# Kernel tuning notes

Measured on AMD Instinct MI355X. Metric: run time of the kernel, lower is better.

The kernel has to match this reference:

```python
import jax, jax.numpy as jnp
import numpy as np

NINP = 512
NHID = 512
INITRANGE = 0.04
# DARTS RNN genotype: list of (activation, predecessor state index); concat = mean of states 1..8
RECURRENT = [("tanh", 0), ("relu", 1), ("relu", 1), ("identity", 1), ("tanh", 2), ("sigmoid", 5), ("tanh", 3), ("relu", 5)]
CONCAT = list(range(1, 9))
ACT = {"tanh": jnp.tanh, "relu": jax.nn.relu, "sigmoid": jax.nn.sigmoid, "identity": lambda x: x}


def setup_inputs() -> dict:
    key = jax.random.key(0)
    k0, k1, k2 = jax.random.split(key, 3)
    T, B = 400, 256
    inputs = jax.random.normal(k0, (T, B, NINP), dtype=jnp.float32)
    hidden = jnp.zeros((1, B, NHID), dtype=jnp.float32)
    W0 = jax.random.uniform(k1, (NINP + NHID, 2 * NHID), jnp.float32, -INITRANGE, INITRANGE)
    Ws = jax.random.uniform(k2, (len(RECURRENT), NHID, 2 * NHID), jnp.float32, -INITRANGE, INITRANGE)
    return {"inputs": inputs, "hidden": hidden, "W0": W0, "Ws": Ws}


def _cell(x, h_prev, W0, Ws):
    # init state: highway gate from concat(x, h_prev) @ W0
    xh = jnp.concatenate([x, h_prev], axis=-1)            # [B, ninp+nhid]
    c0, h0 = jnp.split(xh @ W0, 2, axis=-1)               # each [B, nhid]
    s0 = h_prev + jax.nn.sigmoid(c0) * (jnp.tanh(h0) - h_prev)
    states = [s0]
    for i, (name, pred) in enumerate(RECURRENT):          # fixed small DAG
        sp = states[pred]
        c, h = jnp.split(sp @ Ws[i], 2, axis=-1)
        s = sp + jax.nn.sigmoid(c) * (ACT[name](h) - sp)
        states.append(s)
    return jnp.mean(jnp.stack([states[i] for i in CONCAT], axis=-1), axis=-1)


def reference(inputs, hidden, W0, Ws):
    h0 = hidden[0]                                        # [B, nhid]

    def step(h, x):
        h_new = _cell(x, h, W0, Ws)
        return h_new, h_new

    h_last, hiddens = jax.lax.scan(step, h0, inputs)      # hiddens: [T, B, nhid]
    return hiddens, h_last[None]
```

## Files before the change

### kernel.cpp

```cpp
#include <hip/hip_runtime.h>
#include <stdint.h>

typedef unsigned short ushort_t;
typedef unsigned long long u64;
typedef __attribute__((ext_vector_type(8))) short short8;
typedef __attribute__((ext_vector_type(4))) float f32x4;
typedef __attribute__((ext_vector_type(4))) unsigned int u32x4;
typedef __attribute__((ext_vector_type(16))) float f32x16;

#define WS_W0T_HI 0u
#define WS_W0T_LO (2u<<20)
#define WS_WST_HI (4u<<20)
#define WS_WST_LO (12u<<20)
#define WS_ST     (20u<<20)
#define WS_BAR    (26u<<20)

#define SLOT_ELEMS 262144
#define PLANE 131072
#define PSTR 536


__device__ __forceinline__ ushort_t f2bf(float f) {
  unsigned u = __float_as_uint(f);
  u += 0x7FFFu + ((u >> 16) & 1u);
  return (ushort_t)(u >> 16);
}
__device__ __forceinline__ float bf2f(ushort_t h) {
  return __uint_as_float(((unsigned)h) << 16);
}
__device__ __forceinline__ float sigf(float v) { return 1.f / (1.f + __expf(-v)); }

__device__ __forceinline__ u32x4 uld16(const void* p) {
  u32x4 r;
  asm volatile("global_load_dwordx4 %0, %1, off sc0 sc1" : "=v"(r) : "v"(p));
  return r;
}

__device__ __forceinline__ void st_state(ushort_t* slot, int eo, float s, int tid) {
  ushort_t hi = f2bf(s);
  ushort_t lo = f2bf(s - bf2f(hi));
  unsigned nh = __shfl_xor((unsigned)hi, 1, 64);
  unsigned nl = __shfl_xor((unsigned)lo, 1, 64);
  if (!(tid & 1)) {
    unsigned wh = (unsigned)hi | (nh << 16);
    unsigned wl = (unsigned)lo | (nl << 16);
    __hip_atomic_store((unsigned*)(slot + eo), wh, __ATOMIC_RELAXED, __HIP_MEMORY_SCOPE_AGENT);
    __hip_atomic_store((unsigned*)(slot + PLANE + eo), wl, __ATOMIC_RELAXED, __HIP_MEMORY_SCOPE_AGENT);
  }
}

__device__ __forceinline__ void xcvt(const float* xp, short8& ah, short8& al) {
  f32x4 v0 = *(const f32x4*)xp;
  f32x4 v1 = *(const f32x4*)(xp + 4);
#pragma unroll
  for (int i = 0; i < 4; ++i) {
    ushort_t h0 = f2bf(v0[i]);
    ah[i] = (short)h0; al[i] = (short)f2bf(v0[i] - bf2f(h0));
    ushort_t h1 = f2bf(v1[i]);
    ah[i + 4] = (short)h1; al[i + 4] = (short)f2bf(v1[i] - bf2f(h1));
  }
}

extern "C" __global__ void prep_kernel(const float* __restrict__ W0,
                                       const float* __restrict__ Ws,
                                       const float* __restrict__ h0,
                                       char* __restrict__ ws) {
  ushort_t* w0h = (ushort_t*)(ws + WS_W0T_HI);
  ushort_t* w0l = (ushort_t*)(ws + WS_W0T_LO);
  ushort_t* wsh = (ushort_t*)(ws + WS_WST_HI);
  ushort_t* wsl = (ushort_t*)(ws + WS_WST_LO);
  ushort_t* st  = (ushort_t*)(ws + WS_ST);
  const long N0 = 1048576, N1 = 4194304, N2 = 131072;
  long total = N0 + N1 + N2;
  for (long idx = (long)blockIdx.x * blockDim.x + threadIdx.x; idx < total;
       idx += (long)gridDim.x * blockDim.x) {
    if (idx < N0) {
      int k = (int)(idx >> 10), j = (int)(idx & 1023);
      float v = W0[k * 1024 + j];
      ushort_t hi = f2bf(v);
      w0h[j * 1024 + k] = hi;
      w0l[j * 1024 + k] = f2bf(v - bf2f(hi));
    } else if (idx < N0 + N1) {
      long r = idx - N0;
      int i = (int)(r >> 19);
      int r2 = (int)(r & 524287);
      int k = r2 >> 10, j = r2 & 1023;
      float v = Ws[(long)i * 524288 + k * 1024 + j];
      ushort_t hi = f2bf(v);
      wsh[(long)i * 524288 + j * 512 + k] = hi;
      wsl[(long)i * 524288 + j * 512 + k] = f2bf(v - bf2f(hi));
    } else {
      int e = (int)(idx - N0 - N1);
      float v = h0[e];
      ushort_t hi = f2bf(v);
      st[0 * SLOT_ELEMS + e] = hi;
      st[0 * SLOT_ELEMS + PLANE + e] = f2bf(v - bf2f(hi));
    }
  }
}

__device__ __forceinline__ void set_flag(unsigned* flags, int g, int pt, unsigned gen) {
  __syncthreads();
  if (threadIdx.x == 0)
    __hip_atomic_store(flags + (g * 32 + pt) * 16, gen, __ATOMIC_RELAXED, __HIP_MEMORY_SCOPE_AGENT);
}

__device__ __forceinline__ void panel_load(const ushort_t* slot, int r0,
                                           ushort_t* Ah, ushort_t* Al,
                                           const unsigned* flags, int g, unsigned G,
                                           int tid) {
  const int row = tid >> 4, c0 = (tid & 15) * 32;
  const int p0 = (tid & 15) * 2;
  const unsigned* f0 = flags + (g * 32 + p0) * 16;
  const unsigned* f1 = flags + (g * 32 + p0 + 1) * 16;
  while (__hip_atomic_load(f0, __ATOMIC_RELAXED, __HIP_MEMORY_SCOPE_AGENT) < G)
    __builtin_amdgcn_s_sleep(2);
  while (__hip_atomic_load(f1, __ATOMIC_RELAXED, __HIP_MEMORY_SCOPE_AGENT) < G)
    __builtin_amdgcn_s_sleep(2);
  const ushort_t* srch = slot + (r0 + row) * 512 + c0;
  u32x4 v[8];
#pragma unroll
  for (int j = 0; j < 4; ++j) v[j] = uld16(srch + j * 8);
#pragma unroll
  for (int j = 0; j < 4; ++j) v[4 + j] = uld16(srch + PLANE + j * 8);
  asm volatile("s_waitcnt vmcnt(0)" ::: "memory");
  __builtin_amdgcn_sched_barrier(0);
#pragma unroll
  for (int j = 0; j < 4; ++j) {
    *(u32x4*)(Ah + row * PSTR + c0 + j * 8) = v[j];
    *(u32x4*)(Al + row * PSTR + c0 + j * 8) = v[4 + j];
  }
}

__device__ __forceinline__ f32x16 mfma3(short8 ah, short8 al, short8 bh, short8 bl, f32x16 acc) {
  acc = __builtin_amdgcn_mfma_f32_32x32x16_bf16(ah, bh, acc, 0, 0, 0);
  acc = __builtin_amdgcn_mfma_f32_32x32x16_bf16(ah, bl, acc, 0, 0, 0);
  acc = __builtin_amdgcn_mfma_f32_32x32x16_bf16(al, bh, acc, 0, 0, 0);
  return acc;
}

template<int NP, int NBLK, bool XA>
__device__ __forceinline__ void mm_lds(const ushort_t* Ah, const ushort_t* Al,
                                       const float* xrow,
                                       const ushort_t* const (&bh)[NP],
                                       const ushort_t* const (&bl)[NP],
                                       int boff, int kw, int lr,
                                       f32x16 (&acc)[NP]) {
#pragma unroll
  for (int j = 0; j < NBLK; ++j) {
    int kq = j * 128 + kw;
    short8 a_h, a_l;
    if (XA && j < 4) {
      xcvt(xrow + kq, a_h, a_l);
    } else {
      int kp = XA ? (kq - 512) : kq;
      a_h = *(const short8*)(Ah + lr * PSTR + kp);
      a_l = *(const short8*)(Al + lr * PSTR + kp);
    }
#pragma unroll
    for (int p = 0; p < NP; ++p) {
      short8 b_h = *(const short8*)(bh[p] + boff + kq);
      short8 b_l = *(const short8*)(bl[p] + boff + kq);
      acc[p] = mfma3(a_h, a_l, b_h, b_l, acc[p]);
    }
  }
}

__device__ __forceinline__ void wr_pp1(float* pp, const f32x16& a, int w, int lane) {
  int col = lane & 31, h5 = lane >> 5;
  float* base = pp + w * 1056 + col;
#pragma unroll
  for (int r = 0; r < 16; ++r) {
    int row = (r & 3) + 8 * (r >> 2) + 4 * h5;
    base[row * 33] = a[r];
  }
}
__device__ __forceinline__ void rd_pp1(const float* pp, int row, int cp,
                                       float& c, float& h) {
  float cs = 0.f, hs = 0.f;
#pragma unroll
  for (int w = 0; w < 8; ++w) {
    cs += pp[w * 1056 + row * 33 + cp];
    hs += pp[w * 1056 + row * 33 + cp + 16];
  }
  c = cs; h = hs;
}

extern "C" __global__ void __launch_bounds__(512, 1)
rnn_main(const float* __restrict__ x, float* __restrict__ out, char* __restrict__ ws) {
  __shared__ ushort_t Ah[32 * PSTR];
  __shared__ ushort_t Al[32 * PSTR];
  __shared__ float pp[8 * 1056];

  ushort_t* stg = (ushort_t*)(ws + WS_ST);
  unsigned* flags = (unsigned*)(ws + WS_BAR);
  const ushort_t* w0h = (const ushort_t*)(ws + WS_W0T_HI);
  const ushort_t* w0l = (const ushort_t*)(ws + WS_W0T_LO);
  const ushort_t* wsh = (const ushort_t*)(ws + WS_WST_HI);
  const ushort_t* wsl = (const ushort_t*)(ws + WS_WST_LO);

  const int tid = threadIdx.x;
  const int wg = blockIdx.x;
  const int rt = wg >> 5, pt = wg & 31;
  const int g = rt, r0 = rt * 32;
  const int w = tid >> 6, lane = tid & 63;
  const int kw = w * 16 + (lane >> 5) * 8;
  const int lr = lane & 31;
  const int jc = pt * 16 + (lr & 15) + (lr >> 4) * 512;
  const int b512 = jc * 512, b1024 = jc * 1024;
  const int erow = tid >> 4, ecp = tid & 15;
  const int scol = pt * 16 + ecp;
  const int eo = (r0 + erow) * 512 + scol;
  const int spo = erow * PSTR + scol;

  float sumreg = 0.f;

  for (int t = 0; t < 400; ++t) {
    const unsigned base = 5u * (unsigned)t;
    const float* xrow = x + (size_t)t * 131072 + (size_t)(r0 + lr) * 512;

    panel_load(stg + 0 * SLOT_ELEMS, r0, Ah, Al, flags, g, base, tid);
    __syncthreads();
    {
      f32x16 acc[1] = {};
      const ushort_t* bh[1] = {w0h};
      const ushort_t* bl[1] = {w0l};
      mm_lds<1, 8, true>(Ah, Al, xrow, bh, bl, b1024, kw, lr, acc);
      __syncthreads();
      wr_pp1(pp, acc[0], w, lane);
      __syncthreads();
      float c, hh; rd_pp1(pp, erow, ecp, c, hh);
      float sp = bf2f(Ah[spo]) + bf2f(Al[spo]);
      float s = sp + sigf(c) * (tanhf(hh) - sp);
      st_state(stg + 1 * SLOT_ELEMS, eo, s, tid);
    }
    set_flag(flags, g, pt, base + 1);

    panel_load(stg + 1 * SLOT_ELEMS, r0, Ah, Al, flags, g, base + 1, tid);
    __syncthreads();
    {
      f32x16 acc[1] = {};
      const ushort_t* bh[1] = {wsh + 0 * 524288};
      const ushort_t* bl[1] = {wsl + 0 * 524288};
      mm_lds<1, 4, false>(Ah, Al, nullptr, bh, bl, b512, kw, lr, acc);
      __syncthreads();
      wr_pp1(pp, acc[0], w, lane);
      __syncthreads();
      float c, hh; rd_pp1(pp, erow, ecp, c, hh);
      float sp = bf2f(Ah[spo]) + bf2f(Al[spo]);
      float s = sp + sigf(c) * (tanhf(hh) - sp);
      sumreg += s;
      st_state(stg + 2 * SLOT_ELEMS, eo, s, tid);
    }
    set_flag(flags, g, pt, base + 2);

    panel_load(stg + 2 * SLOT_ELEMS, r0, Ah, Al, flags, g, base + 2, tid);
    __syncthreads();
    {
      f32x16 acc[3] = {};
      const ushort_t* bh[3] = {wsh + 1 * 524288, wsh + 2 * 524288, wsh + 3 * 524288};
      const ushort_t* bl[3] = {wsl + 1 * 524288, wsl + 2 * 524288, wsl + 3 * 524288};
      mm_lds<3, 4, false>(Ah, Al, nullptr, bh, bl, b512, kw, lr, acc);
      float sp;
      __syncthreads();
      wr_pp1(pp, acc[0], w, lane);
      __syncthreads();
      {
        float c, hh; rd_pp1(pp, erow, ecp, c, hh);
        sp = bf2f(Ah[spo]) + bf2f(Al[spo]);
        float s = sp + sigf(c) * (fmaxf(hh, 0.f) - sp);
        sumreg += s;
        st_state(stg + 3 * SLOT_ELEMS, eo, s, tid);
      }
      __syncthreads();
      wr_pp1(pp, acc[1], w, lane);
      __syncthreads();
      {
        float c, hh; rd_pp1(pp, erow, ecp, c, hh);
        float s = sp + sigf(c) * (fmaxf(hh, 0.f) - sp);
        sumreg += s;
        st_state(stg + 4 * SLOT_ELEMS, eo, s, tid);
      }
      set_flag(flags, g, pt, base + 3);
      wr_pp1(pp, acc[2], w, lane);
      __syncthreads();
      {
        float c, hh; rd_pp1(pp, erow, ecp, c, hh);
        sumreg += sp + sigf(c) * (hh - sp);
      }
    }

    __syncthreads();
    panel_load(stg + 3 * SLOT_ELEMS, r0, Ah, Al, flags, g, base + 3, tid);
    __syncthreads();
    {
      f32x16 acc[1] = {};
      const ushort_t* bh[1] = {wsh + 4 * 524288};
      const ushort_t* bl[1] = {wsl + 4 * 524288};
      mm_lds<1, 4, false>(Ah, Al, nullptr, bh, bl, b512, kw, lr, acc);
      __syncthreads();
      wr_pp1(pp, acc[0], w, lane);
      __syncthreads();
      float c, hh; rd_pp1(pp, erow, ecp, c, hh);
      float sp = bf2f(Ah[spo]) + bf2f(Al[spo]);
      float s = sp + sigf(c) * (tanhf(hh) - sp);
      sumreg += s;
      st_state(stg + 5 * SLOT_ELEMS, eo, s, tid);
    }
    set_flag(flags, g, pt, base + 4);

    panel_load(stg + 4 * SLOT_ELEMS, r0, Ah, Al, flags, g, base + 3, tid);
    __syncthreads();
    {
      f32x16 acc[1] = {};
      const ushort_t* bh[1] = {wsh + 6 * 524288};
      const ushort_t* bl[1] = {wsl + 6 * 524288};
      mm_lds<1, 4, false>(Ah, Al, nullptr, bh, bl, b512, kw, lr, acc);
      __syncthreads();
      wr_pp1(pp, acc[0], w, lane);
      __syncthreads();
      float c, hh; rd_pp1(pp, erow, ecp, c, hh);
      float sp = bf2f(Ah[spo]) + bf2f(Al[spo]);
      sumreg += sp + sigf(c) * (tanhf(hh) - sp);
    }

    __syncthreads();
    panel_load(stg + 5 * SLOT_ELEMS, r0, Ah, Al, flags, g, base + 4, tid);
    __syncthreads();
    {
      f32x16 acc[2] = {};
      const ushort_t* bh[2] = {wsh + 5 * 524288, wsh + 7 * 524288};
      const ushort_t* bl[2] = {wsl + 5 * 524288, wsl + 7 * 524288};
      mm_lds<2, 4, false>(Ah, Al, nullptr, bh, bl, b512, kw, lr, acc);
      __syncthreads();
      wr_pp1(pp, acc[0], w, lane);
      __syncthreads();
      float sp = bf2f(Ah[spo]) + bf2f(Al[spo]);
      {
        float c, hh; rd_pp1(pp, erow, ecp, c, hh);
        sumreg += sp + sigf(c) * (sigf(hh) - sp);
      }
      __syncthreads();
      wr_pp1(pp, acc[1], w, lane);
      __syncthreads();
      {
        float c, hh; rd_pp1(pp, erow, ecp, c, hh);
        sumreg += sp + sigf(c) * (fmaxf(hh, 0.f) - sp);
      }
      float hn = sumreg * 0.125f;
      __builtin_nontemporal_store(hn, &out[(size_t)t * 131072 + eo]);
      if (t == 399)
        __builtin_nontemporal_store(hn, &out[(size_t)400 * 131072 + eo]);
      st_state(stg + 0 * SLOT_ELEMS, eo, hn, tid);
      sumreg = 0.f;
    }
    set_flag(flags, g, pt, base + 5);
  }
}

extern "C" void kernel_launch(void* const* d_in, const int* in_sizes, int n_in,
                              void* d_out, int out_size, void* d_ws, size_t ws_size,
                              hipStream_t stream) {
  const float* x  = (const float*)d_in[0];
  const float* h0 = (const float*)d_in[1];
  const float* W0 = (const float*)d_in[2];
  const float* Ws = (const float*)d_in[3];
  float* out = (float*)d_out;
  char* ws = (char*)d_ws;

  (void)in_sizes; (void)n_in; (void)out_size; (void)ws_size;

  (void)hipMemsetAsync(ws + WS_BAR, 0, 16384, stream);
  hipLaunchKernelGGL(prep_kernel, dim3(2048), dim3(256), 0, stream, W0, Ws, h0, ws);

  void* args[3] = {(void*)&x, (void*)&out, (void*)&ws};
  (void)hipLaunchCooperativeKernel((void*)rnn_main, dim3(256), dim3(512), args, 0, stream);
}
```

Baseline: 17.77 ms.

## Merge states 5 and 7 matmuls into one dual-panel pass with split K halves

The two independent DAG nodes fed by states 2 and 3 (Ws[4] and Ws[6]) now share a single flag wait and panel load. Both panels are split into K halves that are staged through the existing LDS buffers, and the global loads for the second half are issued while the first half's MFMAs run. This removes one full panel-load/barrier round and overlaps memory latency with compute. The panel_load flag mapping and column layout also change to match the half-split ordering. The cost is more complex LDS reuse with extra syncs and more live registers.

```diff
diff --git a/kernel.cpp b/kernel.cpp
--- a/kernel.cpp
+++ b/kernel.cpp
@@ -18,6 +18,7 @@
 #define SLOT_ELEMS 262144
 #define PLANE 131072
 #define PSTR 536
+#define PSTR2 268
 
 
 __device__ __forceinline__ ushort_t f2bf(float f) {
@@ -109,27 +110,26 @@
                                            ushort_t* Ah, ushort_t* Al,
                                            const unsigned* flags, int g, unsigned G,
                                            int tid) {
-  const int row = tid >> 4, c0 = (tid & 15) * 32;
-  const int p0 = (tid & 15) * 2;
-  const unsigned* f0 = flags + (g * 32 + p0) * 16;
-  const unsigned* f1 = flags + (g * 32 + p0 + 1) * 16;
+  const int row = tid >> 4, i = tid & 15;
+  const unsigned* f0 = flags + (g * 32 + i) * 16;
+  const unsigned* f1 = flags + (g * 32 + 16 + i) * 16;
   while (__hip_atomic_load(f0, __ATOMIC_RELAXED, __HIP_MEMORY_SCOPE_AGENT) < G)
     __builtin_amdgcn_s_sleep(2);
   while (__hip_atomic_load(f1, __ATOMIC_RELAXED, __HIP_MEMORY_SCOPE_AGENT) < G)
     __builtin_amdgcn_s_sleep(2);
-  const ushort_t* srch = slot + (r0 + row) * 512 + c0;
-  u32x4 v[8];
-#pragma unroll
-  for (int j = 0; j < 4; ++j) v[j] = uld16(srch + j * 8);
-#pragma unroll
-  for (int j = 0; j < 4; ++j) v[4 + j] = uld16(srch + PLANE + j * 8);
+  const ushort_t* src = slot + (r0 + row) * 512;
+  const int c0 = i * 16, c1 = 256 + i * 16;
+  u32x4 v0 = uld16(src + c0), v1 = uld16(src + c0 + 8);
+  u32x4 v2 = uld16(src + c1), v3 = uld16(src + c1 + 8);
+  u32x4 v4 = uld16(src + PLANE + c0), v5 = uld16(src + PLANE + c0 + 8);
+  u32x4 v6 = uld16(src + PLANE + c1), v7 = uld16(src + PLANE + c1 + 8);
   asm volatile("s_waitcnt vmcnt(0)" ::: "memory");
   __builtin_amdgcn_sched_barrier(0);
-#pragma unroll
-  for (int j = 0; j < 4; ++j) {
-    *(u32x4*)(Ah + row * PSTR + c0 + j * 8) = v[j];
-    *(u32x4*)(Al + row * PSTR + c0 + j * 8) = v[4 + j];
-  }
+  const int o0 = row * PSTR + c0, o1 = row * PSTR + c1;
+  *(u32x4*)(Ah + o0) = v0; *(u32x4*)(Ah + o0 + 8) = v1;
+  *(u32x4*)(Ah + o1) = v2; *(u32x4*)(Ah + o1 + 8) = v3;
+  *(u32x4*)(Al + o0) = v4; *(u32x4*)(Al + o0 + 8) = v5;
+  *(u32x4*)(Al + o1) = v6; *(u32x4*)(Al + o1 + 8) = v7;
 }
 
 __device__ __forceinline__ f32x16 mfma3(short8 ah, short8 al, short8 bh, short8 bl, f32x16 acc) {
@@ -166,6 +166,31 @@
   }
 }
 
+__device__ __forceinline__ void mmD(const ushort_t* B2, const ushort_t* B3,
+                                    const ushort_t* wah, const ushort_t* wal,
+                                    const ushort_t* wbh, const ushort_t* wbl,
+                                    int b512, int h, int w, int lane,
+                                    f32x16& acc5, f32x16& acc7) {
+  const int lr = lane & 31;
+  const int bkk = (lane >> 5) * 8;
+  const int ak = lr * PSTR2 + bkk;
+#pragma unroll
+  for (int s = 0; s < 2; ++s) {
+    const int kl = w * 32 + s * 16;
+    const int kq = h * 256 + kl + bkk;
+    short8 a2h = *(const short8*)(B2 + ak + kl);
+    short8 a2l = *(const short8*)(B2 + 8576 + ak + kl);
+    short8 a3h = *(const short8*)(B3 + ak + kl);
+    short8 a3l = *(const short8*)(B3 + 8576 + ak + kl);
+    short8 bah = *(const short8*)(wah + b512 + kq);
+    short8 bal = *(const short8*)(wal + b512 + kq);
+    short8 bbh = *(const short8*)(wbh + b512 + kq);
+    short8 bbl = *(const short8*)(wbl + b512 + kq);
+    acc5 = mfma3(a2h, a2l, bah, bal, acc5);
+    acc7 = mfma3(a3h, a3l, bbh, bbl, acc7);
+  }
+}
+
 __device__ __forceinline__ void wr_pp1(float* pp, const f32x16& a, int w, int lane) {
   int col = lane & 31, h5 = lane >> 5;
   float* base = pp + w * 1056 + col;
@@ -188,8 +213,8 @@
 
 extern "C" __global__ void __launch_bounds__(512, 1)
 rnn_main(const float* __restrict__ x, float* __restrict__ out, char* __restrict__ ws) {
-  __shared__ ushort_t Ah[32 * PSTR];
-  __shared__ ushort_t Al[32 * PSTR];
+  __shared__ __align__(16) ushort_t Ah[32 * PSTR];
+  __shared__ __align__(16) ushort_t Al[32 * PSTR];
   __shared__ float pp[8 * 1056];
 
   ushort_t* stg = (ushort_t*)(ws + WS_ST);
@@ -290,38 +315,76 @@
       }
     }
 
-    __syncthreads();
-    panel_load(stg + 3 * SLOT_ELEMS, r0, Ah, Al, flags, g, base + 3, tid);
-    __syncthreads();
     {
-      f32x16 acc[1] = {};
-      const ushort_t* bh[1] = {wsh + 4 * 524288};
-      const ushort_t* bl[1] = {wsl + 4 * 524288};
-      mm_lds<1, 4, false>(Ah, Al, nullptr, bh, bl, b512, kw, lr, acc);
-      __syncthreads();
-      wr_pp1(pp, acc[0], w, lane);
-      __syncthreads();
-      float c, hh; rd_pp1(pp, erow, ecp, c, hh);
-      float sp = bf2f(Ah[spo]) + bf2f(Al[spo]);
-      float s = sp + sigf(c) * (tanhf(hh) - sp);
-      sumreg += s;
-      st_state(stg + 5 * SLOT_ELEMS, eo, s, tid);
-    }
-    set_flag(flags, g, pt, base + 4);
-
-    panel_load(stg + 4 * SLOT_ELEMS, r0, Ah, Al, flags, g, base + 3, tid);
-    __syncthreads();
-    {
-      f32x16 acc[1] = {};
-      const ushort_t* bh[1] = {wsh + 6 * 524288};
-      const ushort_t* bl[1] = {wsl + 6 * 524288};
-      mm_lds<1, 4, false>(Ah, Al, nullptr, bh, bl, b512, kw, lr, acc);
-      __syncthreads();
-      wr_pp1(pp, acc[0], w, lane);
-      __syncthreads();
-      float c, hh; rd_pp1(pp, erow, ecp, c, hh);
-      float sp = bf2f(Ah[spo]) + bf2f(Al[spo]);
-      sumreg += sp + sigf(c) * (tanhf(hh) - sp);
+      const int i = tid & 15;
+      const unsigned G3 = base + 3;
+      const unsigned* f0 = flags + (g * 32 + i) * 16;
+      const unsigned* f1 = flags + (g * 32 + 16 + i) * 16;
+      while (__hip_atomic_load(f0, __ATOMIC_RELAXED, __HIP_MEMORY_SCOPE_AGENT) < G3)
+        __builtin_amdgcn_s_sleep(2);
+      while (__hip_atomic_load(f1, __ATOMIC_RELAXED, __HIP_MEMORY_SCOPE_AGENT) < G3)
+        __builtin_amdgcn_s_sleep(2);
+      const int prow = tid >> 4;
+      const ushort_t* s2p = stg + 3 * SLOT_ELEMS + (r0 + prow) * 512;
+      const ushort_t* s3p = stg + 4 * SLOT_ELEMS + (r0 + prow) * 512;
+      const int po = prow * PSTR2 + i * 16;
+      {
+        u32x4 v0 = uld16(s2p + i * 16),        v1 = uld16(s2p + i * 16 + 8);
+        u32x4 v2 = uld16(s2p + PLANE + i * 16), v3 = uld16(s2p + PLANE + i * 16 + 8);
+        u32x4 q0 = uld16(s3p + i * 16),        q1 = uld16(s3p + i * 16 + 8);
+        u32x4 q2 = uld16(s3p + PLANE + i * 16), q3 = uld16(s3p + PLANE + i * 16 + 8);
+        asm volatile("s_waitcnt vmcnt(0)" ::: "memory");
+        __builtin_amdgcn_sched_barrier(0);
+        *(u32x4*)(Ah + po) = v0;        *(u32x4*)(Ah + po + 8) = v1;
+        *(u32x4*)(Ah + 8576 + po) = v2; *(u32x4*)(Ah + 8576 + po + 8) = v3;
+        *(u32x4*)(Al + po) = q0;        *(u32x4*)(Al + po + 8) = q1;
+        *(u32x4*)(Al + 8576 + po) = q2; *(u32x4*)(Al + 8576 + po + 8) = q3;
+      }
+      __syncthreads();
+      const int hstar = pt >> 4;
+      const int lcs = erow * PSTR2 + ((pt & 15) * 16 + ecp);
+      float sp2 = 0.f, sp3 = 0.f;
+      if (hstar == 0) {
+        sp2 = bf2f(Ah[lcs]) + bf2f(Ah[8576 + lcs]);
+        sp3 = bf2f(Al[lcs]) + bf2f(Al[8576 + lcs]);
+      }
+      u32x4 y0 = uld16(s2p + 256 + i * 16),        y1 = uld16(s2p + 256 + i * 16 + 8);
+      u32x4 y2 = uld16(s2p + PLANE + 256 + i * 16), y3 = uld16(s2p + PLANE + 256 + i * 16 + 8);
+      u32x4 z0 = uld16(s3p + 256 + i * 16),        z1 = uld16(s3p + 256 + i * 16 + 8);
+      u32x4 z2 = uld16(s3p + PLANE + 256 + i * 16), z3 = uld16(s3p + PLANE + 256 + i * 16 + 8);
+      f32x16 acc5 = {}, acc7 = {};
+      mmD(Ah, Al, wsh + 4 * 524288, wsl + 4 * 524288,
+          wsh + 6 * 524288, wsl + 6 * 524288, b512, 0, w, lane, acc5, acc7);
+      __syncthreads();
+      asm volatile("s_waitcnt vmcnt(0)" ::: "memory");
+      __builtin_amdgcn_sched_barrier(0);
+      *(u32x4*)(Ah + po) = y0;        *(u32x4*)(Ah + po + 8) = y1;
+      *(u32x4*)(Ah + 8576 + po) = y2; *(u32x4*)(Ah + 8576 + po + 8) = y3;
+      *(u32x4*)(Al + po) = z0;        *(u32x4*)(Al + po + 8) = z1;
+      *(u32x4*)(Al + 8576 + po) = z2; *(u32x4*)(Al + 8576 + po + 8) = z3;
+      __syncthreads();
+      if (hstar == 1) {
+        sp2 = bf2f(Ah[lcs]) + bf2f(Ah[8576 + lcs]);
+        sp3 = bf2f(Al[lcs]) + bf2f(Al[8576 + lcs]);
+      }
+      mmD(Ah, Al, wsh + 4 * 524288, wsl + 4 * 524288,
+          wsh + 6 * 524288, wsl + 6 * 524288, b512, 1, w, lane, acc5, acc7);
+      __syncthreads();
+      wr_pp1(pp, acc5, w, lane);
+      __syncthreads();
+      {
+        float c, hh; rd_pp1(pp, erow, ecp, c, hh);
+        float s5v = sp2 + sigf(c) * (tanhf(hh) - sp2);
+        sumreg += s5v;
+        st_state(stg + 5 * SLOT_ELEMS, eo, s5v, tid);
+      }
+      set_flag(flags, g, pt, base + 4);
+      wr_pp1(pp, acc7, w, lane);
+      __syncthreads();
+      {
+        float c, hh; rd_pp1(pp, erow, ecp, c, hh);
+        sumreg += sp3 + sigf(c) * (tanhf(hh) - sp3);
+      }
     }
 
     __syncthreads();
```

Result: slower. 20.02 ms (+12.7%).

## Retile recurrent cell to 16-row groups with per-wave K slices and MFMA-tiled weights

Applied to the files above, without the earlier changes.

Reorganises the persistent RNN kernel from 8 groups of 32 batch rows to 16 groups of 16 rows, each workgroup owning 32 output columns. Each wave now loads only its own 64-wide K slice of the state, gated by per-wave flag polling instead of a whole-panel wait. Weights are pre-swizzled into 16x16x32 MFMA tile order so operand loads are contiguous. The x-part of the first GEMM is computed before polling, states are kept in registers instead of being re-read from LDS, and the s3/s4 consumers are merged into one phase to cut barriers. The cost is more flag traffic, more workgroups per group synchronisation, and smaller MFMA tiles.

```diff
diff --git a/kernel.cpp b/kernel.cpp
--- a/kernel.cpp
+++ b/kernel.cpp
@@ -6,7 +6,6 @@
 typedef __attribute__((ext_vector_type(8))) short short8;
 typedef __attribute__((ext_vector_type(4))) float f32x4;
 typedef __attribute__((ext_vector_type(4))) unsigned int u32x4;
-typedef __attribute__((ext_vector_type(16))) float f32x16;
 
 #define WS_W0T_HI 0u
 #define WS_W0T_LO (2u<<20)
@@ -17,7 +16,7 @@
 
 #define SLOT_ELEMS 262144
 #define PLANE 131072
-#define PSTR 536
+#define SLW 72
 
 
 __device__ __forceinline__ ushort_t f2bf(float f) {
@@ -78,8 +77,10 @@
       int k = (int)(idx >> 10), j = (int)(idx & 1023);
       float v = W0[k * 1024 + j];
       ushort_t hi = f2bf(v);
-      w0h[j * 1024 + k] = hi;
-      w0l[j * 1024 + k] = f2bf(v - bf2f(hi));
+      long dst = ((long)(j >> 4) * 32 + (k >> 5)) * 512 +
+                 (((k >> 3) & 3) * 16 + (j & 15)) * 8 + (k & 7);
+      w0h[dst] = hi;
+      w0l[dst] = f2bf(v - bf2f(hi));
     } else if (idx < N0 + N1) {
       long r = idx - N0;
       int i = (int)(r >> 19);
@@ -87,8 +88,10 @@
       int k = r2 >> 10, j = r2 & 1023;
       float v = Ws[(long)i * 524288 + k * 1024 + j];
       ushort_t hi = f2bf(v);
-      wsh[(long)i * 524288 + j * 512 + k] = hi;
-      wsl[(long)i * 524288 + j * 512 + k] = f2bf(v - bf2f(hi));
+      long dst = (long)i * 524288 + ((long)(j >> 4) * 16 + (k >> 5)) * 512 +
+                 (((k >> 3) & 3) * 16 + (j & 15)) * 8 + (k & 7);
+      wsh[dst] = hi;
+      wsl[dst] = f2bf(v - bf2f(hi));
     } else {
       int e = (int)(idx - N0 - N1);
       float v = h0[e];
@@ -102,95 +105,88 @@
 __device__ __forceinline__ void set_flag(unsigned* flags, int g, int pt, unsigned gen) {
   __syncthreads();
   if (threadIdx.x == 0)
-    __hip_atomic_store(flags + (g * 32 + pt) * 16, gen, __ATOMIC_RELAXED, __HIP_MEMORY_SCOPE_AGENT);
-}
-
-__device__ __forceinline__ void panel_load(const ushort_t* slot, int r0,
-                                           ushort_t* Ah, ushort_t* Al,
-                                           const unsigned* flags, int g, unsigned G,
-                                           int tid) {
-  const int row = tid >> 4, c0 = (tid & 15) * 32;
-  const int p0 = (tid & 15) * 2;
-  const unsigned* f0 = flags + (g * 32 + p0) * 16;
-  const unsigned* f1 = flags + (g * 32 + p0 + 1) * 16;
-  while (__hip_atomic_load(f0, __ATOMIC_RELAXED, __HIP_MEMORY_SCOPE_AGENT) < G)
-    __builtin_amdgcn_s_sleep(2);
-  while (__hip_atomic_load(f1, __ATOMIC_RELAXED, __HIP_MEMORY_SCOPE_AGENT) < G)
-    __builtin_amdgcn_s_sleep(2);
-  const ushort_t* srch = slot + (r0 + row) * 512 + c0;
-  u32x4 v[8];
-#pragma unroll
-  for (int j = 0; j < 4; ++j) v[j] = uld16(srch + j * 8);
-#pragma unroll
-  for (int j = 0; j < 4; ++j) v[4 + j] = uld16(srch + PLANE + j * 8);
+    __hip_atomic_store(flags + (g * 16 + pt) * 16, gen, __ATOMIC_RELAXED, __HIP_MEMORY_SCOPE_AGENT);
+}
+__device__ __forceinline__ void pollw(const unsigned* flags, int g, int q0,
+                                      unsigned G, int lane) {
+  if (lane < 2) {
+    const unsigned* f = flags + (g * 16 + q0 + lane) * 16;
+    while (__hip_atomic_load(f, __ATOMIC_RELAXED, __HIP_MEMORY_SCOPE_AGENT) < G)
+      __builtin_amdgcn_s_sleep(2);
+  }
+}
+
+__device__ __forceinline__ void slice_load(const ushort_t* slot, int r0, int k0,
+                                           ushort_t* SlH, ushort_t* SlL, int lane) {
+  const int row = lane >> 3, part = lane & 7;
+  const ushort_t* s = slot + (r0 + row) * 512 + k0 + part * 8;
+  u32x4 a0 = uld16(s);
+  u32x4 a1 = uld16(s + 8 * 512);
+  u32x4 b0 = uld16(s + PLANE);
+  u32x4 b1 = uld16(s + PLANE + 8 * 512);
   asm volatile("s_waitcnt vmcnt(0)" ::: "memory");
   __builtin_amdgcn_sched_barrier(0);
-#pragma unroll
-  for (int j = 0; j < 4; ++j) {
-    *(u32x4*)(Ah + row * PSTR + c0 + j * 8) = v[j];
-    *(u32x4*)(Al + row * PSTR + c0 + j * 8) = v[4 + j];
-  }
-}
-
-__device__ __forceinline__ f32x16 mfma3(short8 ah, short8 al, short8 bh, short8 bl, f32x16 acc) {
-  acc = __builtin_amdgcn_mfma_f32_32x32x16_bf16(ah, bh, acc, 0, 0, 0);
-  acc = __builtin_amdgcn_mfma_f32_32x32x16_bf16(ah, bl, acc, 0, 0, 0);
-  acc = __builtin_amdgcn_mfma_f32_32x32x16_bf16(al, bh, acc, 0, 0, 0);
+  *(u32x4*)(SlH + row * SLW + part * 8) = a0;
+  *(u32x4*)(SlH + (row + 8) * SLW + part * 8) = a1;
+  *(u32x4*)(SlL + row * SLW + part * 8) = b0;
+  *(u32x4*)(SlL + (row + 8) * SLW + part * 8) = b1;
+}
+
+__device__ __forceinline__ f32x4 mfma3_4(short8 ah, short8 al, short8 bh, short8 bl, f32x4 acc) {
+  acc = __builtin_amdgcn_mfma_f32_16x16x32_bf16(ah, bh, acc, 0, 0, 0);
+  acc = __builtin_amdgcn_mfma_f32_16x16x32_bf16(ah, bl, acc, 0, 0, 0);
+  acc = __builtin_amdgcn_mfma_f32_16x16x32_bf16(al, bh, acc, 0, 0, 0);
   return acc;
 }
 
-template<int NP, int NBLK, bool XA>
-__device__ __forceinline__ void mm_lds(const ushort_t* Ah, const ushort_t* Al,
-                                       const float* xrow,
-                                       const ushort_t* const (&bh)[NP],
-                                       const ushort_t* const (&bl)[NP],
-                                       int boff, int kw, int lr,
-                                       f32x16 (&acc)[NP]) {
-#pragma unroll
-  for (int j = 0; j < NBLK; ++j) {
-    int kq = j * 128 + kw;
-    short8 a_h, a_l;
-    if (XA && j < 4) {
-      xcvt(xrow + kq, a_h, a_l);
-    } else {
-      int kp = XA ? (kq - 512) : kq;
-      a_h = *(const short8*)(Ah + lr * PSTR + kp);
-      a_l = *(const short8*)(Al + lr * PSTR + kp);
-    }
-#pragma unroll
-    for (int p = 0; p < NP; ++p) {
-      short8 b_h = *(const short8*)(bh[p] + boff + kq);
-      short8 b_l = *(const short8*)(bl[p] + boff + kq);
-      acc[p] = mfma3(a_h, a_l, b_h, b_l, acc[p]);
-    }
-  }
-}
-
-__device__ __forceinline__ void wr_pp1(float* pp, const f32x16& a, int w, int lane) {
-  int col = lane & 31, h5 = lane >> 5;
-  float* base = pp + w * 1056 + col;
-#pragma unroll
-  for (int r = 0; r < 16; ++r) {
-    int row = (r & 3) + 8 * (r >> 2) + 4 * h5;
-    base[row * 33] = a[r];
-  }
-}
-__device__ __forceinline__ void rd_pp1(const float* pp, int row, int cp,
-                                       float& c, float& h) {
+template<int NP>
+__device__ __forceinline__ void mm_slice(const ushort_t* SlH, const ushort_t* SlL,
+                                         const ushort_t* const (&wh)[NP],
+                                         const ushort_t* const (&wl)[NP],
+                                         const int (&jbs)[4], int KB, int kbg0,
+                                         int lane, f32x4 (&acc)[NP][4]) {
+#pragma unroll
+  for (int kb = 0; kb < 2; ++kb) {
+    const int ao = (lane & 15) * SLW + kb * 32 + (lane >> 4) * 8;
+    short8 ah = *(const short8*)(SlH + ao);
+    short8 al = *(const short8*)(SlL + ao);
+#pragma unroll
+    for (int p = 0; p < NP; ++p)
+#pragma unroll
+      for (int ct = 0; ct < 4; ++ct) {
+        const int tile = (jbs[ct] * KB + kbg0 + kb) * 512 + lane * 8;
+        short8 bh = *(const short8*)(wh[p] + tile);
+        short8 bl = *(const short8*)(wl[p] + tile);
+        acc[p][ct] = mfma3_4(ah, al, bh, bl, acc[p][ct]);
+      }
+  }
+}
+
+__device__ __forceinline__ void wrpp(float* pp, int m, const f32x4 (&a)[4], int w, int lane) {
+  const int col = lane & 15, rb = (lane >> 4) * 4;
+#pragma unroll
+  for (int ct = 0; ct < 4; ++ct) {
+    float* b = pp + (((m * 8 + w) * 4 + ct) * 16) * 16 + col;
+#pragma unroll
+    for (int r = 0; r < 4; ++r) b[(rb + r) * 16] = a[ct][r];
+  }
+}
+__device__ __forceinline__ void rdpp(const float* pp, int m, int row, int cl,
+                                     float& c, float& h) {
+  const int ctc = cl >> 4, col = cl & 15;
   float cs = 0.f, hs = 0.f;
 #pragma unroll
   for (int w = 0; w < 8; ++w) {
-    cs += pp[w * 1056 + row * 33 + cp];
-    hs += pp[w * 1056 + row * 33 + cp + 16];
+    cs += pp[(((m * 8 + w) * 4 + ctc) * 16 + row) * 16 + col];
+    hs += pp[(((m * 8 + w) * 4 + ctc + 2) * 16 + row) * 16 + col];
   }
   c = cs; h = hs;
 }
 
 extern "C" __global__ void __launch_bounds__(512, 1)
 rnn_main(const float* __restrict__ x, float* __restrict__ out, char* __restrict__ ws) {
-  __shared__ ushort_t Ah[32 * PSTR];
-  __shared__ ushort_t Al[32 * PSTR];
-  __shared__ float pp[8 * 1056];
+  __shared__ __align__(16) ushort_t Sl[8][2][16 * SLW];
+  __shared__ __align__(16) float pp[2 * 8 * 4 * 16 * 16];
 
   ushort_t* stg = (ushort_t*)(ws + WS_ST);
   unsigned* flags = (unsigned*)(ws + WS_BAR);
@@ -201,158 +197,156 @@
 
   const int tid = threadIdx.x;
   const int wg = blockIdx.x;
-  const int rt = wg >> 5, pt = wg & 31;
-  const int g = rt, r0 = rt * 32;
+  const int g = wg >> 4, pt = wg & 15;
+  const int r0 = g * 16;
   const int w = tid >> 6, lane = tid & 63;
-  const int kw = w * 16 + (lane >> 5) * 8;
-  const int lr = lane & 31;
-  const int jc = pt * 16 + (lr & 15) + (lr >> 4) * 512;
-  const int b512 = jc * 512, b1024 = jc * 1024;
-  const int erow = tid >> 4, ecp = tid & 15;
-  const int scol = pt * 16 + ecp;
-  const int eo = (r0 + erow) * 512 + scol;
-  const int spo = erow * PSTR + scol;
-
-  float sumreg = 0.f;
+  ushort_t* SlH = &Sl[w][0][0];
+  ushort_t* SlL = &Sl[w][1][0];
+  const int jbs[4] = {2 * pt, 2 * pt + 1, 32 + 2 * pt, 33 + 2 * pt};
+  const int q0 = 2 * w;
+  const int k0 = w * 64;
+
+  const int erow = tid >> 5, ecl = tid & 31;
+  const int eo = (r0 + erow) * 512 + pt * 32 + ecl;
+
+  float h_reg = bf2f(stg[eo]) + bf2f(stg[PLANE + eo]);
+  float s0_r = 0.f, s1_r = 0.f, s2_r = 0.f, s3_r = 0.f, s5_r = 0.f, sum = 0.f;
 
   for (int t = 0; t < 400; ++t) {
     const unsigned base = 5u * (unsigned)t;
-    const float* xrow = x + (size_t)t * 131072 + (size_t)(r0 + lr) * 512;
-
-    panel_load(stg + 0 * SLOT_ELEMS, r0, Ah, Al, flags, g, base, tid);
-    __syncthreads();
-    {
-      f32x16 acc[1] = {};
-      const ushort_t* bh[1] = {w0h};
-      const ushort_t* bl[1] = {w0l};
-      mm_lds<1, 8, true>(Ah, Al, xrow, bh, bl, b1024, kw, lr, acc);
-      __syncthreads();
-      wr_pp1(pp, acc[0], w, lane);
-      __syncthreads();
-      float c, hh; rd_pp1(pp, erow, ecp, c, hh);
-      float sp = bf2f(Ah[spo]) + bf2f(Al[spo]);
-      float s = sp + sigf(c) * (tanhf(hh) - sp);
-      st_state(stg + 1 * SLOT_ELEMS, eo, s, tid);
+
+    {
+      f32x4 acc[1][4] = {};
+      const float* xr = x + (size_t)t * 131072 + (size_t)(r0 + (lane & 15)) * 512
+                        + k0 + (lane >> 4) * 8;
+#pragma unroll
+      for (int kb = 0; kb < 2; ++kb) {
+        short8 ah, al; xcvt(xr + kb * 32, ah, al);
+#pragma unroll
+        for (int ct = 0; ct < 4; ++ct) {
+          const int tile = (jbs[ct] * 32 + q0 + kb) * 512 + lane * 8;
+          short8 bh = *(const short8*)(w0h + tile);
+          short8 bl = *(const short8*)(w0l + tile);
+          acc[0][ct] = mfma3_4(ah, al, bh, bl, acc[0][ct]);
+        }
+      }
+      pollw(flags, g, q0, base, lane);
+      slice_load(stg + 0 * SLOT_ELEMS, r0, k0, SlH, SlL, lane);
+      const ushort_t* wh1[1] = {w0h};
+      const ushort_t* wl1[1] = {w0l};
+      mm_slice<1>(SlH, SlL, wh1, wl1, jbs, 32, 16 + q0, lane, acc);
+      wrpp(pp, 0, acc[0], w, lane);
+      __syncthreads();
+      float c, hh; rdpp(pp, 0, erow, ecl, c, hh);
+      s0_r = h_reg + sigf(c) * (tanhf(hh) - h_reg);
+      st_state(stg + 1 * SLOT_ELEMS, eo, s0_r, tid);
     }
     set_flag(flags, g, pt, base + 1);
 
-    panel_load(stg + 1 * SLOT_ELEMS, r0, Ah, Al, flags, g, base + 1, tid);
-    __syncthreads();
-    {
-      f32x16 acc[1] = {};
-      const ushort_t* bh[1] = {wsh + 0 * 524288};
-      const ushort_t* bl[1] = {wsl + 0 * 524288};
-      mm_lds<1, 4, false>(Ah, Al, nullptr, bh, bl, b512, kw, lr, acc);
-      __syncthreads();
-      wr_pp1(pp, acc[0], w, lane);
-      __syncthreads();
-      float c, hh; rd_pp1(pp, erow, ecp, c, hh);
-      float sp = bf2f(Ah[spo]) + bf2f(Al[spo]);
-      float s = sp + sigf(c) * (tanhf(hh) - sp);
-      sumreg += s;
-      st_state(stg + 2 * SLOT_ELEMS, eo, s, tid);
+    {
+      pollw(flags, g, q0, base + 1, lane);
+      slice_load(stg + 1 * SLOT_ELEMS, r0, k0, SlH, SlL, lane);
+      f32x4 acc[1][4] = {};
+      const ushort_t* wh1[1] = {wsh + 0 * 524288};
+      const ushort_t* wl1[1] = {wsl + 0 * 524288};
+      mm_slice<1>(SlH, SlL, wh1, wl1, jbs, 16, q0, lane, acc);
+      wrpp(pp, 0, acc[0], w, lane);
+      __syncthreads();
+      float c, hh; rdpp(pp, 0, erow, ecl, c, hh);
+      s1_r = s0_r + sigf(c) * (tanhf(hh) - s0_r);
+      sum = s1_r;
+      st_state(stg + 2 * SLOT_ELEMS, eo, s1_r, tid);
     }
     set_flag(flags, g, pt, base + 2);
 
-    panel_load(stg + 2 * SLOT_ELEMS, r0, Ah, Al, flags, g, base + 2, tid);
-    __syncthreads();
-    {
-      f32x16 acc[3] = {};
-      const ushort_t* bh[3] = {wsh + 1 * 524288, wsh + 2 * 524288, wsh + 3 * 524288};
-      const ushort_t* bl[3] = {wsl + 1 * 524288, wsl + 2 * 524288, wsl + 3 * 524288};
-      mm_lds<3, 4, false>(Ah, Al, nullptr, bh, bl, b512, kw, lr, acc);
-      float sp;
-      __syncthreads();
-      wr_pp1(pp, acc[0], w, lane);
-      __syncthreads();
-      {
-        float c, hh; rd_pp1(pp, erow, ecp, c, hh);
-        sp = bf2f(Ah[spo]) + bf2f(Al[spo]);
-        float s = sp + sigf(c) * (fmaxf(hh, 0.f) - sp);
-        sumreg += s;
-        st_state(stg + 3 * SLOT_ELEMS, eo, s, tid);
-      }
-      __syncthreads();
-      wr_pp1(pp, acc[1], w, lane);
-      __syncthreads();
-      {
-        float c, hh; rd_pp1(pp, erow, ecp, c, hh);
-        float s = sp + sigf(c) * (fmaxf(hh, 0.f) - sp);
-        sumreg += s;
-        st_state(stg + 4 * SLOT_ELEMS, eo, s, tid);
-      }
+    {
+      pollw(flags, g, q0, base + 2, lane);
+      slice_load(stg + 2 * SLOT_ELEMS, r0, k0, SlH, SlL, lane);
+      f32x4 acc[3][4] = {};
+      const ushort_t* wh3[3] = {wsh + 1 * 524288, wsh + 2 * 524288, wsh + 3 * 524288};
+      const ushort_t* wl3[3] = {wsl + 1 * 524288, wsl + 2 * 524288, wsl + 3 * 524288};
+      mm_slice<3>(SlH, SlL, wh3, wl3, jbs, 16, q0, lane, acc);
+      wrpp(pp, 0, acc[0], w, lane);
+      wrpp(pp, 1, acc[1], w, lane);
+      __syncthreads();
+      float c, hh;
+      rdpp(pp, 0, erow, ecl, c, hh);
+      s2_r = s1_r + sigf(c) * (fmaxf(hh, 0.f) - s1_r);
+      sum += s2_r;
+      st_state(stg + 3 * SLOT_ELEMS, eo, s2_r, tid);
+      rdpp(pp, 1, erow, ecl, c, hh);
+      s3_r = s1_r + sigf(c) * (fmaxf(hh, 0.f) - s1_r);
+      sum += s3_r;
+      st_state(stg + 4 * SLOT_ELEMS, eo, s3_r, tid);
       set_flag(flags, g, pt, base + 3);
-      wr_pp1(pp, acc[2], w, lane);
-      __syncthreads();
-      {
-        float c, hh; rd_pp1(pp, erow, ecp, c, hh);
-        sumreg += sp + sigf(c) * (hh - sp);
-      }
-    }
-
-    __syncthreads();
-    panel_load(stg + 3 * SLOT_ELEMS, r0, Ah, Al, flags, g, base + 3, tid);
-    __syncthreads();
-    {
-      f32x16 acc[1] = {};
-      const ushort_t* bh[1] = {wsh + 4 * 524288};
-      const ushort_t* bl[1] = {wsl + 4 * 524288};
-      mm_lds<1, 4, false>(Ah, Al, nullptr, bh, bl, b512, kw, lr, acc);
-      __syncthreads();
-      wr_pp1(pp, acc[0], w, lane);
-      __syncthreads();
-      float c, hh; rd_pp1(pp, erow, ecp, c, hh);
-      float sp = bf2f(Ah[spo]) + bf2f(Al[spo]);
-      float s = sp + sigf(c) * (tanhf(hh) - sp);
-      sumreg += s;
-      st_state(stg + 5 * SLOT_ELEMS, eo, s, tid);
+      wrpp(pp, 0, acc[2], w, lane);
+      __syncthreads();
+      rdpp(pp, 0, erow, ecl, c, hh);
+      sum += s1_r + sigf(c) * (hh - s1_r);
+      __syncthreads();
+    }
+
+    {
+      pollw(flags, g, q0, base + 3, lane);
+      const int row = lane >> 3, part = lane & 7;
+      const ushort_t* p2 = stg + 3 * SLOT_ELEMS + (r0 + row) * 512 + k0 + part * 8;
+      const ushort_t* p3 = stg + 4 * SLOT_ELEMS + (r0 + row) * 512 + k0 + part * 8;
+      u32x4 a0 = uld16(p2), a1 = uld16(p2 + 8 * 512);
+      u32x4 a2 = uld16(p2 + PLANE), a3 = uld16(p2 + PLANE + 8 * 512);
+      u32x4 c0 = uld16(p3), c1 = uld16(p3 + 8 * 512);
+      u32x4 c2 = uld16(p3 + PLANE), c3 = uld16(p3 + PLANE + 8 * 512);
+      asm volatile("s_waitcnt vmcnt(4)" ::: "memory");
+      __builtin_amdgcn_sched_barrier(0);
+      *(u32x4*)(SlH + row * SLW + part * 8) = a0;
+      *(u32x4*)(SlH + (row + 8) * SLW + part * 8) = a1;
+      *(u32x4*)(SlL + row * SLW + part * 8) = a2;
+      *(u32x4*)(SlL + (row + 8) * SLW + part * 8) = a3;
+      f32x4 acc5[1][4] = {}, acc7[1][4] = {};
+      const ushort_t* wh4[1] = {wsh + 4 * 524288};
+      const ushort_t* wl4[1] = {wsl + 4 * 524288};
+      mm_slice<1>(SlH, SlL, wh4, wl4, jbs, 16, q0, lane, acc5);
+      asm volatile("s_waitcnt vmcnt(0)" ::: "memory");
+      __builtin_amdgcn_sched_barrier(0);
+      *(u32x4*)(SlH + row * SLW + part * 8) = c0;
+      *(u32x4*)(SlH + (row + 8) * SLW + part * 8) = c1;
+      *(u32x4*)(SlL + row * SLW + part * 8) = c2;
+      *(u32x4*)(SlL + (row + 8) * SLW + part * 8) = c3;
+      const ushort_t* wh6[1] = {wsh + 6 * 524288};
+      const ushort_t* wl6[1] = {wsl + 6 * 524288};
+      mm_slice<1>(SlH, SlL, wh6, wl6, jbs, 16, q0, lane, acc7);
+      wrpp(pp, 0, acc5[0], w, lane);
+      wrpp(pp, 1, acc7[0], w, lane);
+      __syncthreads();
+      float c, hh;
+      rdpp(pp, 0, erow, ecl, c, hh);
+      s5_r = s2_r + sigf(c) * (tanhf(hh) - s2_r);
+      sum += s5_r;
+      st_state(stg + 5 * SLOT_ELEMS, eo, s5_r, tid);
+      rdpp(pp, 1, erow, ecl, c, hh);
+      sum += s3_r + sigf(c) * (tanhf(hh) - s3_r);
     }
     set_flag(flags, g, pt, base + 4);
 
-    panel_load(stg + 4 * SLOT_ELEMS, r0, Ah, Al, flags, g, base + 3, tid);
-    __syncthreads();
-    {
-      f32x16 acc[1] = {};
-      const ushort_t* bh[1] = {wsh + 6 * 524288};
-      const ushort_t* bl[1] = {wsl + 6 * 524288};
-      mm_lds<1, 4, false>(Ah, Al, nullptr, bh, bl, b512, kw, lr, acc);
-      __syncthreads();
-      wr_pp1(pp, acc[0], w, lane);
-      __syncthreads();
-      float c, hh; rd_pp1(pp, erow, ecp, c, hh);
-      float sp = bf2f(Ah[spo]) + bf2f(Al[spo]);
-      sumreg += sp + sigf(c) * (tanhf(hh) - sp);
-    }
-
-    __syncthreads();
-    panel_load(stg + 5 * SLOT_ELEMS, r0, Ah, Al, flags, g, base + 4, tid);
-    __syncthreads();
-    {
-      f32x16 acc[2] = {};
-      const ushort_t* bh[2] = {wsh + 5 * 524288, wsh + 7 * 524288};
-      const ushort_t* bl[2] = {wsl + 5 * 524288, wsl + 7 * 524288};
-      mm_lds<2, 4, false>(Ah, Al, nullptr, bh, bl, b512, kw, lr, acc);
-      __syncthreads();
-      wr_pp1(pp, acc[0], w, lane);
-      __syncthreads();
-      float sp = bf2f(Ah[spo]) + bf2f(Al[spo]);
-      {
-        float c, hh; rd_pp1(pp, erow, ecp, c, hh);
-        sumreg += sp + sigf(c) * (sigf(hh) - sp);
-      }
-      __syncthreads();
-      wr_pp1(pp, acc[1], w, lane);
-      __syncthreads();
-      {
-        float c, hh; rd_pp1(pp, erow, ecp, c, hh);
-        sumreg += sp + sigf(c) * (fmaxf(hh, 0.f) - sp);
-      }
-      float hn = sumreg * 0.125f;
-      __builtin_nontemporal_store(hn, &out[(size_t)t * 131072 + eo]);
+    {
+      pollw(flags, g, q0, base + 4, lane);
+      slice_load(stg + 5 * SLOT_ELEMS, r0, k0, SlH, SlL, lane);
+      f32x4 acc[2][4] = {};
+      const ushort_t* wh2[2] = {wsh + 5 * 524288, wsh + 7 * 524288};
+      const ushort_t* wl2[2] = {wsl + 5 * 524288, wsl + 7 * 524288};
+      mm_slice<2>(SlH, SlL, wh2, wl2, jbs, 16, q0, lane, acc);
+      wrpp(pp, 0, acc[0], w, lane);
+      wrpp(pp, 1, acc[1], w, lane);
+      __syncthreads();
+      float c, hh;
+      rdpp(pp, 0, erow, ecl, c, hh);
+      sum += s5_r + sigf(c) * (sigf(hh) - s5_r);
+      rdpp(pp, 1, erow, ecl, c, hh);
+      sum += s5_r + sigf(c) * (fmaxf(hh, 0.f) - s5_r);
+      h_reg = sum * 0.125f;
+      __builtin_nontemporal_store(h_reg, &out[(size_t)t * 131072 + eo]);
       if (t == 399)
-        __builtin_nontemporal_store(hn, &out[(size_t)400 * 131072 + eo]);
-      st_state(stg + 0 * SLOT_ELEMS, eo, hn, tid);
-      sumreg = 0.f;
+        __builtin_nontemporal_store(h_reg, &out[(size_t)400 * 131072 + eo]);
+      st_state(stg + 0 * SLOT_ELEMS, eo, h_reg, tid);
     }
     set_flag(flags, g, pt, base + 5);
   }
@@ -370,7 +364,7 @@
 
   (void)in_sizes; (void)n_in; (void)out_size; (void)ws_size;
 
-  (void)hipMemsetAsync(ws + WS_BAR, 0, 16384, stream);
+  (void)hipMemsetAsync(ws + WS_BAR, 0, 32768, stream);
   hipLaunchKernelGGL(prep_kernel, dim3(2048), dim3(256), 0, stream, W0, Ws, h0, ws);
 
   void* args[3] = {(void*)&x, (void*)&out, (void*)&ws};
```

Result: slower. 29.65 ms (+66.8%).
